# Kernel optimization log

Measured on AMD Instinct MI355X. Metric: run time of the kernel, lower is better.

The kernel has to match this reference:

```python
import jax, jax.numpy as jnp
import numpy as np

B, T, C, H = 4, 2048, 1024, 16
D = C // H  # head_dim = 64
SCALE = D ** -0.5


def setup_inputs() -> dict:
    key = jax.random.key(0)
    ks = jax.random.split(key, 5)
    s = C ** -0.5
    return {
        "x": jax.random.normal(ks[0], (B, T, C), dtype=jnp.float32),
        "W_qkv": jax.random.normal(ks[1], (C, 3 * C), dtype=jnp.float32) * s,
        "b_qkv": jnp.zeros((3 * C,), dtype=jnp.float32),
        "W_out": jax.random.normal(ks[2], (C, C), dtype=jnp.float32) * s,
        "b_out": jnp.zeros((C,), dtype=jnp.float32),
    }


def reference(x, W_qkv, b_qkv, W_out, b_out):
    Bx, Tx, Cx = x.shape
    qkv = x @ W_qkv + b_qkv                      # [B,T,3C]
    qkv = qkv.reshape(Bx, Tx, 3, H, D)
    q, k, v = qkv[:, :, 0], qkv[:, :, 1], qkv[:, :, 2]  # [B,T,H,D]
    # scores [B,H,T,T]
    scores = jnp.einsum("bthd,bshd->bhts", q, k) * SCALE
    causal = jnp.tril(jnp.ones((Tx, Tx), dtype=bool))
    scores = jnp.where(causal[None, None], scores, -jnp.inf)
    probs = jax.nn.softmax(scores, axis=-1)
    out = jnp.einsum("bhts,bshd->bthd", probs, v).reshape(Bx, Tx, Cx)
    return out @ W_out + b_out
```

## Files before the change

### kernel.cpp

```cpp
#include <hip/hip_runtime.h>
#include <cstdint>
#include <cstddef>

#define B_ 4
#define T_ 2048
#define C_ 1024
#define H_ 16
#define D_ 64
#define SCALE_ 0.125f

typedef _Float16 f16;
typedef f16 f16x4 __attribute__((ext_vector_type(4)));
typedef f16 f16x8 __attribute__((ext_vector_type(8)));
typedef float f32x4 __attribute__((ext_vector_type(4)));

__device__ __forceinline__ void async_ld16(const void* g, void* l) {
  __builtin_amdgcn_global_load_lds(
      (const __attribute__((address_space(1))) void*)g,
      (__attribute__((address_space(3))) void*)l,
      16, 0, 0);
}

__global__ void k_prep(const float* __restrict__ x, f16* __restrict__ xh,
                       const float* __restrict__ Wqkv, f16* __restrict__ WqkvT,
                       const float* __restrict__ Wout, f16* __restrict__ WoutT)
{
  __shared__ float tile[32][33];
  const int bx = blockIdx.x, t = threadIdx.x;
  if (bx < 8192) {
    int i = bx * 256 + t;
    float4 v = ((const float4*)x)[i];
    f16x4 h;
    h.x = (f16)v.x; h.y = (f16)v.y; h.z = (f16)v.z; h.w = (f16)v.w;
    ((f16x4*)xh)[i] = h;
    return;
  }
  const float* in; f16* out; int K, N, nt, kt;
  if (bx < 8192 + 3072) {
    int idx = bx - 8192; in = Wqkv; out = WqkvT; K = 1024; N = 3072;
    nt = idx % 96; kt = idx / 96;
  } else {
    int idx = bx - 11264; in = Wout; out = WoutT; K = 1024; N = 1024;
    nt = idx % 32; kt = idx / 32;
  }
  int tx = t & 31, ty = t >> 5;
  int k0 = kt * 32, n0 = nt * 32;
#pragma unroll
  for (int i = 0; i < 32; i += 8)
    tile[ty + i][tx] = in[(size_t)(k0 + ty + i) * N + n0 + tx];
  __syncthreads();
#pragma unroll
  for (int i = 0; i < 32; i += 8)
    out[(size_t)(n0 + ty + i) * K + k0 + tx] = (f16)tile[tx][ty + i];
}

__global__ void k_vtrans(const f16* __restrict__ QKV, f16* __restrict__ Vt) {
  __shared__ f16 tile[32][33];
  int tx = threadIdx.x & 31, ty = threadIdx.x >> 5;
  int t0 = blockIdx.x * 32, d0 = blockIdx.y * 32;
  int bh = blockIdx.z, b = bh >> 4, h = bh & 15;
#pragma unroll
  for (int i = 0; i < 32; i += 8)
    tile[ty + i][tx] = QKV[(size_t)(b * T_ + t0 + ty + i) * (3 * C_) + 2 * C_ + h * D_ + d0 + tx];
  __syncthreads();
#pragma unroll
  for (int i = 0; i < 32; i += 8)
    Vt[((size_t)bh * D_ + d0 + ty + i) * T_ + t0 + tx] = tile[tx][ty + i];
}

__global__ __launch_bounds__(256, 3)
void k_gemm_bt(const f16* __restrict__ A, const f16* __restrict__ Bt,
               const float* __restrict__ bias, f16* __restrict__ Ch,
               float* __restrict__ Cf, int M, int N, int K)
{
  __shared__ __align__(16) f16 As[2][128 * 32];
  __shared__ __align__(16) f16 Bs[2][128 * 32];
  const int t = threadIdx.x;
  const int wave = t >> 6, lane = t & 63, lr = lane & 15, quad = lane >> 4;
  const int row0 = blockIdx.y * 128, col0 = blockIdx.x * 128;
  const int wm = (wave >> 1) * 64, wn = (wave & 1) * 64;

  f32x4 acc[4][4] = {};

  const int sw = ((t & 3) ^ ((t >> 4) & 3)) * 8;
  const f16* gA = A + (size_t)(row0 + (t >> 2)) * K + sw;
  const f16* gB = Bt + (size_t)(col0 + (t >> 2)) * K + sw;
  const size_t rowskip = (size_t)64 * K;
  const int rc = (quad ^ (lr >> 2)) * 8;

  {
    f16* lA = As[0] + wave * 512;
    f16* lB = Bs[0] + wave * 512;
    async_ld16(gA,           lA);
    async_ld16(gA + rowskip, lA + 2048);
    async_ld16(gB,           lB);
    async_ld16(gB + rowskip, lB + 2048);
  }

  const int iters = K >> 5;
  for (int it = 0; it < iters; ++it) {
    __syncthreads();
    const int buf = it & 1;
    if (it + 1 < iters) {
      const int k0 = (it + 1) * 32;
      f16* lA = As[buf ^ 1] + wave * 512;
      f16* lB = Bs[buf ^ 1] + wave * 512;
      async_ld16(gA + k0,           lA);
      async_ld16(gA + rowskip + k0, lA + 2048);
      async_ld16(gB + k0,           lB);
      async_ld16(gB + rowskip + k0, lB + 2048);
    }
    const f16* As_ = As[buf];
    const f16* Bs_ = Bs[buf];

    f16x8 af[4], bf[4];
#pragma unroll
    for (int i = 0; i < 4; ++i) {
      af[i] = *(const f16x8*)&As_[(wm + i * 16 + lr) * 32 + rc];
      bf[i] = *(const f16x8*)&Bs_[(wn + i * 16 + lr) * 32 + rc];
    }
#pragma unroll
    for (int mi = 0; mi < 4; ++mi)
#pragma unroll
      for (int ni = 0; ni < 4; ++ni)
        acc[mi][ni] = __builtin_amdgcn_mfma_f32_16x16x32_f16(af[mi], bf[ni], acc[mi][ni], 0, 0, 0);
  }

#pragma unroll
  for (int mi = 0; mi < 4; ++mi) {
#pragma unroll
    for (int ni = 0; ni < 4; ++ni) {
      int col = col0 + wn + ni * 16 + lr;
      float bv = bias[col];
#pragma unroll
      for (int r = 0; r < 4; ++r) {
        int row = row0 + wm + mi * 16 + quad * 4 + r;
        float v = acc[mi][ni][r] + bv;
        if (Ch) Ch[(size_t)row * N + col] = (f16)v;
        else    Cf[(size_t)row * N + col] = v;
      }
    }
  }
}

__global__ __launch_bounds__(256, 4)
void k_flash(const f16* __restrict__ QKV, const f16* __restrict__ Vt, f16* __restrict__ O)
{
  __shared__ __align__(16) f16 Ks[2][64 * 64];
  __shared__ __align__(16) f16 Vs[2][64 * 64];
  __shared__ __align__(16) f16 Ps[4][16 * 64];

  const int a = blockIdx.x, bh = blockIdx.y;
  const int b = bh >> 4, h = bh & 15;
  const int qtA = a, qtB = 31 - a;
  const int t = threadIdx.x, wave = t >> 6, lane = t & 63, lr = lane & 15, quad = lane >> 4;
  const int lr3 = lr & 7;
  const int c0 = quad ^ lr3;
  const int c1 = c0 ^ 4;

  const f16 scl = (f16)0.125f;
  const f16* qpA = QKV + (size_t)(b * T_ + qtA * 64 + wave * 16 + lr) * 3072 + h * 64;
  const f16* qpB = QKV + (size_t)(b * T_ + qtB * 64 + wave * 16 + lr) * 3072 + h * 64;
  f16x8 qA0 = *(const f16x8*)(qpA + quad * 8)      * scl;
  f16x8 qA1 = *(const f16x8*)(qpA + 32 + quad * 8) * scl;
  f16x8 qB0 = *(const f16x8*)(qpB + quad * 8)      * scl;
  f16x8 qB1 = *(const f16x8*)(qpB + 32 + quad * 8) * scl;

  float lA_[4] = {0.f, 0.f, 0.f, 0.f};
  float lB_[4] = {0.f, 0.f, 0.f, 0.f};
  f32x4 oA[4] = {}, oB[4] = {};

  const int sw = ((t & 7) ^ ((t >> 3) & 7)) * 8;
  const f16* gK = QKV + (size_t)(b * T_ + (t >> 3)) * 3072 + 1024 + h * 64 + sw;
  const f16* gV = Vt + ((size_t)bh * 64 + (t >> 3)) * T_ + sw;

  f16* myP = Ps[wave];
  f16* pw0 = myP + (quad * 4) * 64 + ((0 ^ quad) << 4) + lr;
  f16* pw1 = myP + (quad * 4) * 64 + ((1 ^ quad) << 4) + lr;
  f16* pw2 = myP + (quad * 4) * 64 + ((2 ^ quad) << 4) + lr;
  f16* pw3 = myP + (quad * 4) * 64 + ((3 ^ quad) << 4) + lr;
  const f16* pr0 = myP + lr * 64 + ((((quad >> 1))     ^ (lr >> 2)) << 4) + ((quad & 1) << 3);
  const f16* pr1 = myP + lr * 64 + ((((quad >> 1) ^ 2) ^ (lr >> 2)) << 4) + ((quad & 1) << 3);

  const int last = qtB;

  {
    f16* lK = Ks[0] + wave * 512;
    f16* lV = Vs[0] + wave * 512;
    async_ld16(gK,                     lK);
    async_ld16(gK + (size_t)32 * 3072, lK + 2048);
    async_ld16(gV,                     lV);
    async_ld16(gV + (size_t)32 * T_,   lV + 2048);
  }

  for (int kt = 0; kt <= last; ++kt) {
    __syncthreads();
    const int buf = kt & 1;
    if (kt < last) {
      const f16* gk = gK + (size_t)((kt + 1) * 64) * 3072;
      const f16* gv = gV + (kt + 1) * 64;
      f16* lK = Ks[buf ^ 1] + wave * 512;
      f16* lV = Vs[buf ^ 1] + wave * 512;
      async_ld16(gk,                     lK);
      async_ld16(gk + (size_t)32 * 3072, lK + 2048);
      async_ld16(gv,                     lV);
      async_ld16(gv + (size_t)32 * T_,   lV + 2048);
    }
    const f16* K_ = Ks[buf];
    const f16* V_ = Vs[buf];
    const bool actA = (kt <= qtA);

    {
      f32x4 s4[4];
#pragma unroll
      for (int ni = 0; ni < 4; ++ni) {
        const f16* kr = K_ + (ni * 16 + lr) * 64;
        f16x8 k0 = *(const f16x8*)(kr + c0 * 8);
        f16x8 k1 = *(const f16x8*)(kr + c1 * 8);
        f32x4 z = {};
        z = __builtin_amdgcn_mfma_f32_16x16x32_f16(qB0, k0, z, 0, 0, 0);
        z = __builtin_amdgcn_mfma_f32_16x16x32_f16(qB1, k1, z, 0, 0, 0);
        s4[ni] = z;
      }
      if (kt == qtB) {
        const int rloc = wave * 16 + quad * 4;
#pragma unroll
        for (int r = 0; r < 4; ++r) {
#pragma unroll
          for (int ni = 0; ni < 4; ++ni)
            if (ni * 16 + lr > rloc + r) s4[ni][r] = -1e30f;
        }
      }
#pragma unroll
      for (int r = 0; r < 4; ++r) {
        float e0 = __expf(s4[0][r]), e1 = __expf(s4[1][r]);
        float e2 = __expf(s4[2][r]), e3 = __expf(s4[3][r]);
        lB_[r] += (e0 + e1) + (e2 + e3);
        pw0[r * 64] = (f16)e0; pw1[r * 64] = (f16)e1;
        pw2[r * 64] = (f16)e2; pw3[r * 64] = (f16)e3;
      }
      f16x8 pB0 = *(const f16x8*)pr0;
      f16x8 pB1 = *(const f16x8*)pr1;
#pragma unroll
      for (int ni = 0; ni < 4; ++ni) {
        const f16* vr = V_ + (ni * 16 + lr) * 64;
        f16x8 v0 = *(const f16x8*)(vr + c0 * 8);
        f16x8 v1 = *(const f16x8*)(vr + c1 * 8);
        oB[ni] = __builtin_amdgcn_mfma_f32_16x16x32_f16(pB0, v0, oB[ni], 0, 0, 0);
        oB[ni] = __builtin_amdgcn_mfma_f32_16x16x32_f16(pB1, v1, oB[ni], 0, 0, 0);
      }
    }

    if (actA) {
      f32x4 s4[4];
#pragma unroll
      for (int ni = 0; ni < 4; ++ni) {
        const f16* kr = K_ + (ni * 16 + lr) * 64;
        f16x8 k0 = *(const f16x8*)(kr + c0 * 8);
        f16x8 k1 = *(const f16x8*)(kr + c1 * 8);
        f32x4 z = {};
        z = __builtin_amdgcn_mfma_f32_16x16x32_f16(qA0, k0, z, 0, 0, 0);
        z = __builtin_amdgcn_mfma_f32_16x16x32_f16(qA1, k1, z, 0, 0, 0);
        s4[ni] = z;
      }
      if (kt == qtA) {
        const int rloc = wave * 16 + quad * 4;
#pragma unroll
        for (int r = 0; r < 4; ++r) {
#pragma unroll
          for (int ni = 0; ni < 4; ++ni)
            if (ni * 16 + lr > rloc + r) s4[ni][r] = -1e30f;
        }
      }
#pragma unroll
      for (int r = 0; r < 4; ++r) {
        float e0 = __expf(s4[0][r]), e1 = __expf(s4[1][r]);
        float e2 = __expf(s4[2][r]), e3 = __expf(s4[3][r]);
        lA_[r] += (e0 + e1) + (e2 + e3);
        pw0[r * 64] = (f16)e0; pw1[r * 64] = (f16)e1;
        pw2[r * 64] = (f16)e2; pw3[r * 64] = (f16)e3;
      }
      f16x8 pA0 = *(const f16x8*)pr0;
      f16x8 pA1 = *(const f16x8*)pr1;
#pragma unroll
      for (int ni = 0; ni < 4; ++ni) {
        const f16* vr = V_ + (ni * 16 + lr) * 64;
        f16x8 v0 = *(const f16x8*)(vr + c0 * 8);
        f16x8 v1 = *(const f16x8*)(vr + c1 * 8);
        oA[ni] = __builtin_amdgcn_mfma_f32_16x16x32_f16(pA0, v0, oA[ni], 0, 0, 0);
        oA[ni] = __builtin_amdgcn_mfma_f32_16x16x32_f16(pA1, v1, oA[ni], 0, 0, 0);
      }
    }
  }

#pragma unroll
  for (int r = 0; r < 4; ++r) {
    float la = lA_[r], lb = lB_[r];
#pragma unroll
    for (int off = 1; off < 16; off <<= 1) {
      la += __shfl_xor(la, off, 64);
      lb += __shfl_xor(lb, off, 64);
    }
    const int rowA = qtA * 64 + wave * 16 + quad * 4 + r;
    const int rowB = qtB * 64 + wave * 16 + quad * 4 + r;
    float invA = 1.f / la;
    float invB = 1.f / lb;
#pragma unroll
    for (int ni = 0; ni < 4; ++ni) {
      O[(size_t)(b * T_ + rowA) * C_ + h * 64 + ni * 16 + lr] = (f16)(oA[ni][r] * invA);
      O[(size_t)(b * T_ + rowB) * C_ + h * 64 + ni * 16 + lr] = (f16)(oB[ni][r] * invB);
    }
  }
}

extern "C" void kernel_launch(void* const* d_in, const int* in_sizes, int n_in,
                              void* d_out, int out_size, void* d_ws, size_t ws_size,
                              hipStream_t stream)
{
  const float* x    = (const float*)d_in[0];
  const float* Wqkv = (const float*)d_in[1];
  const float* bqkv = (const float*)d_in[2];
  const float* Wout = (const float*)d_in[3];
  const float* bout = (const float*)d_in[4];
  float* out = (float*)d_out;

  f16* xh    = (f16*)d_ws;
  f16* WqkvT = xh + (size_t)8192 * 1024;
  f16* WoutT = WqkvT + (size_t)3072 * 1024;
  f16* QKV   = WoutT + (size_t)1024 * 1024;
  f16* VtG   = QKV + (size_t)8192 * 3072;
  f16* Oh    = VtG + (size_t)64 * 64 * 2048;

  k_prep<<<12288, 256, 0, stream>>>(x, xh, Wqkv, WqkvT, Wout, WoutT);

  k_gemm_bt<<<dim3(3072 / 128, 8192 / 128), 256, 0, stream>>>(
      xh, WqkvT, bqkv, QKV, nullptr, 8192, 3072, 1024);

  k_vtrans<<<dim3(T_ / 32, D_ / 32, B_ * H_), 256, 0, stream>>>(QKV, VtG);

  k_flash<<<dim3(16, B_ * H_), 256, 0, stream>>>(QKV, VtG, Oh);

  k_gemm_bt<<<dim3(1024 / 128, 8192 / 128), 256, 0, stream>>>(
      Oh, WoutT, bout, nullptr, out, 8192, 1024, 1024);
}
```

Before: 274.3 us.

## Fuse V transpose into QKV GEMM epilogue and load GEMM operands directly from global

Drops the separate V-transpose kernel by having the QKV GEMM write V columns straight into the transposed Vt layout in its epilogue. The GEMM main loop also stops staging tiles through LDS with async loads. Each wave now loads its MFMA fragments directly from global memory into registers, using a two-stage register double buffer over K. This saves a launch and a round trip of V through memory. In exchange, operand reuse across waves via shared memory is lost, so global/L2 traffic rises and the Vt stores become strided and uncoalesced.

After: 406.9 us. +48.3%, slower.

```diff
diff --git a/kernel.cpp b/kernel.cpp
--- a/kernel.cpp
+++ b/kernel.cpp
@@ -54,90 +54,86 @@
     out[(size_t)(n0 + ty + i) * K + k0 + tx] = (f16)tile[tx][ty + i];
 }
 
-__global__ void k_vtrans(const f16* __restrict__ QKV, f16* __restrict__ Vt) {
-  __shared__ f16 tile[32][33];
-  int tx = threadIdx.x & 31, ty = threadIdx.x >> 5;
-  int t0 = blockIdx.x * 32, d0 = blockIdx.y * 32;
-  int bh = blockIdx.z, b = bh >> 4, h = bh & 15;
-#pragma unroll
-  for (int i = 0; i < 32; i += 8)
-    tile[ty + i][tx] = QKV[(size_t)(b * T_ + t0 + ty + i) * (3 * C_) + 2 * C_ + h * D_ + d0 + tx];
-  __syncthreads();
-#pragma unroll
-  for (int i = 0; i < 32; i += 8)
-    Vt[((size_t)bh * D_ + d0 + ty + i) * T_ + t0 + tx] = tile[tx][ty + i];
-}
-
 __global__ __launch_bounds__(256, 3)
 void k_gemm_bt(const f16* __restrict__ A, const f16* __restrict__ Bt,
                const float* __restrict__ bias, f16* __restrict__ Ch,
-               float* __restrict__ Cf, int M, int N, int K)
+               float* __restrict__ Cf, f16* __restrict__ VtOut,
+               int M, int N, int K)
 {
-  __shared__ __align__(16) f16 As[2][128 * 32];
-  __shared__ __align__(16) f16 Bs[2][128 * 32];
   const int t = threadIdx.x;
   const int wave = t >> 6, lane = t & 63, lr = lane & 15, quad = lane >> 4;
   const int row0 = blockIdx.y * 128, col0 = blockIdx.x * 128;
   const int wm = (wave >> 1) * 64, wn = (wave & 1) * 64;
 
+  const f16* pa = A  + (size_t)(row0 + wm + lr) * K + quad * 8;
+  const f16* pb = Bt + (size_t)(col0 + wn + lr) * K + quad * 8;
+  const size_t rs = (size_t)16 * K;
+
   f32x4 acc[4][4] = {};
-
-  const int sw = ((t & 3) ^ ((t >> 4) & 3)) * 8;
-  const f16* gA = A + (size_t)(row0 + (t >> 2)) * K + sw;
-  const f16* gB = Bt + (size_t)(col0 + (t >> 2)) * K + sw;
-  const size_t rowskip = (size_t)64 * K;
-  const int rc = (quad ^ (lr >> 2)) * 8;
-
-  {
-    f16* lA = As[0] + wave * 512;
-    f16* lB = Bs[0] + wave * 512;
-    async_ld16(gA,           lA);
-    async_ld16(gA + rowskip, lA + 2048);
-    async_ld16(gB,           lB);
-    async_ld16(gB + rowskip, lB + 2048);
-  }
-
-  const int iters = K >> 5;
-  for (int it = 0; it < iters; ++it) {
-    __syncthreads();
-    const int buf = it & 1;
-    if (it + 1 < iters) {
-      const int k0 = (it + 1) * 32;
-      f16* lA = As[buf ^ 1] + wave * 512;
-      f16* lB = Bs[buf ^ 1] + wave * 512;
-      async_ld16(gA + k0,           lA);
-      async_ld16(gA + rowskip + k0, lA + 2048);
-      async_ld16(gB + k0,           lB);
-      async_ld16(gB + rowskip + k0, lB + 2048);
-    }
-    const f16* As_ = As[buf];
-    const f16* Bs_ = Bs[buf];
-
-    f16x8 af[4], bf[4];
+  f16x8 a0[4], b0[4], a1[4], b1[4];
+
+#pragma unroll
+  for (int i = 0; i < 4; ++i) {
+    a0[i] = *(const f16x8*)(pa + i * rs);
+    b0[i] = *(const f16x8*)(pb + i * rs);
+  }
+
+  for (int k0 = 0; k0 < K; k0 += 64) {
 #pragma unroll
     for (int i = 0; i < 4; ++i) {
-      af[i] = *(const f16x8*)&As_[(wm + i * 16 + lr) * 32 + rc];
-      bf[i] = *(const f16x8*)&Bs_[(wn + i * 16 + lr) * 32 + rc];
+      a1[i] = *(const f16x8*)(pa + i * rs + k0 + 32);
+      b1[i] = *(const f16x8*)(pb + i * rs + k0 + 32);
     }
 #pragma unroll
     for (int mi = 0; mi < 4; ++mi)
 #pragma unroll
       for (int ni = 0; ni < 4; ++ni)
-        acc[mi][ni] = __builtin_amdgcn_mfma_f32_16x16x32_f16(af[mi], bf[ni], acc[mi][ni], 0, 0, 0);
-  }
-
-#pragma unroll
-  for (int mi = 0; mi < 4; ++mi) {
+        acc[mi][ni] = __builtin_amdgcn_mfma_f32_16x16x32_f16(a0[mi], b0[ni], acc[mi][ni], 0, 0, 0);
+    if (k0 + 64 < K) {
+#pragma unroll
+      for (int i = 0; i < 4; ++i) {
+        a0[i] = *(const f16x8*)(pa + i * rs + k0 + 64);
+        b0[i] = *(const f16x8*)(pb + i * rs + k0 + 64);
+      }
+    }
+#pragma unroll
+    for (int mi = 0; mi < 4; ++mi)
+#pragma unroll
+      for (int ni = 0; ni < 4; ++ni)
+        acc[mi][ni] = __builtin_amdgcn_mfma_f32_16x16x32_f16(a1[mi], b1[ni], acc[mi][ni], 0, 0, 0);
+  }
+
+  if (VtOut != nullptr && col0 >= 2048) {
 #pragma unroll
     for (int ni = 0; ni < 4; ++ni) {
-      int col = col0 + wn + ni * 16 + lr;
-      float bv = bias[col];
-#pragma unroll
-      for (int r = 0; r < 4; ++r) {
-        int row = row0 + wm + mi * 16 + quad * 4 + r;
-        float v = acc[mi][ni][r] + bv;
-        if (Ch) Ch[(size_t)row * N + col] = (f16)v;
-        else    Cf[(size_t)row * N + col] = v;
+      const int cb = col0 + wn + ni * 16 - 2048;
+      const int h = cb >> 6;
+      const int dd = (cb & 63) + lr;
+      const float bv = bias[2048 + cb + lr];
+#pragma unroll
+      for (int mi = 0; mi < 4; ++mi) {
+#pragma unroll
+        for (int r = 0; r < 4; ++r) {
+          const int row = row0 + wm + mi * 16 + quad * 4 + r;
+          const int bb = row >> 11, tt = row & 2047;
+          VtOut[((size_t)(bb * 16 + h) * 64 + dd) * T_ + tt] = (f16)(acc[mi][ni][r] + bv);
+        }
+      }
+    }
+  } else {
+#pragma unroll
+    for (int mi = 0; mi < 4; ++mi) {
+#pragma unroll
+      for (int ni = 0; ni < 4; ++ni) {
+        int col = col0 + wn + ni * 16 + lr;
+        float bv = bias[col];
+#pragma unroll
+        for (int r = 0; r < 4; ++r) {
+          int row = row0 + wm + mi * 16 + quad * 4 + r;
+          float v = acc[mi][ni][r] + bv;
+          if (Ch) Ch[(size_t)row * N + col] = (f16)v;
+          else    Cf[(size_t)row * N + col] = v;
+        }
       }
     }
   }
@@ -334,12 +330,10 @@
   k_prep<<<12288, 256, 0, stream>>>(x, xh, Wqkv, WqkvT, Wout, WoutT);
 
   k_gemm_bt<<<dim3(3072 / 128, 8192 / 128), 256, 0, stream>>>(
-      xh, WqkvT, bqkv, QKV, nullptr, 8192, 3072, 1024);
-
-  k_vtrans<<<dim3(T_ / 32, D_ / 32, B_ * H_), 256, 0, stream>>>(QKV, VtG);
+      xh, WqkvT, bqkv, QKV, nullptr, VtG, 8192, 3072, 1024);
 
   k_flash<<<dim3(16, B_ * H_), 256, 0, stream>>>(QKV, VtG, Oh);
 
   k_gemm_bt<<<dim3(1024 / 128, 8192 / 128), 256, 0, stream>>>(
-      Oh, WoutT, bout, nullptr, out, 8192, 1024, 1024);
-}
+      Oh, WoutT, bout, nullptr, out, nullptr, 8192, 1024, 1024);
+}
```

## Fuse V transpose into QKV GEMM epilogue and enlarge tile to 256x128

Applied to the files above, without the earlier changes.

The QKV projection now uses a new GEMM kernel with 256x128 tiles (8x4 MFMA accumulators per wave) instead of 128x128, and blocks covering the V columns write their output directly in transposed [bh][d][t] layout. This removes the separate V-transpose kernel launch and its extra read and write of V. The cost is scattered 2-byte transposed stores in the epilogue, plus more registers per thread that may lower occupancy, and fewer blocks (768 vs 1536) in the grid.

Measured after the change: 261.8 us. 4.6% less time.

```diff
diff --git a/kernel.cpp b/kernel.cpp
--- a/kernel.cpp
+++ b/kernel.cpp
@@ -54,24 +54,106 @@
     out[(size_t)(n0 + ty + i) * K + k0 + tx] = (f16)tile[tx][ty + i];
 }
 
-__global__ void k_vtrans(const f16* __restrict__ QKV, f16* __restrict__ Vt) {
-  __shared__ f16 tile[32][33];
-  int tx = threadIdx.x & 31, ty = threadIdx.x >> 5;
-  int t0 = blockIdx.x * 32, d0 = blockIdx.y * 32;
-  int bh = blockIdx.z, b = bh >> 4, h = bh & 15;
-#pragma unroll
-  for (int i = 0; i < 32; i += 8)
-    tile[ty + i][tx] = QKV[(size_t)(b * T_ + t0 + ty + i) * (3 * C_) + 2 * C_ + h * D_ + d0 + tx];
-  __syncthreads();
-#pragma unroll
-  for (int i = 0; i < 32; i += 8)
-    Vt[((size_t)bh * D_ + d0 + ty + i) * T_ + t0 + tx] = tile[tx][ty + i];
+__global__ __launch_bounds__(256, 3)
+void k_gemm256(const f16* __restrict__ A, const f16* __restrict__ Bt,
+               const float* __restrict__ bias, f16* __restrict__ Ch,
+               f16* __restrict__ VtOut, int M, int N, int K)
+{
+  __shared__ __align__(16) f16 As[2][256 * 32];
+  __shared__ __align__(16) f16 Bs[2][128 * 32];
+  const int t = threadIdx.x;
+  const int wave = t >> 6, lane = t & 63, lr = lane & 15, quad = lane >> 4;
+  const int row0 = blockIdx.y * 256, col0 = blockIdx.x * 128;
+  const int wm = (wave >> 1) * 128, wn = (wave & 1) * 64;
+
+  f32x4 acc[8][4] = {};
+
+  const int sw = ((t & 3) ^ ((t >> 4) & 3)) * 8;
+  const f16* gA = A + (size_t)(row0 + (t >> 2)) * K + sw;
+  const f16* gB = Bt + (size_t)(col0 + (t >> 2)) * K + sw;
+  const size_t rowskip = (size_t)64 * K;
+  const int rc = (quad ^ (lr >> 2)) * 8;
+
+  {
+    f16* lA = As[0] + wave * 512;
+    f16* lB = Bs[0] + wave * 512;
+    async_ld16(gA,                lA);
+    async_ld16(gA + rowskip,      lA + 2048);
+    async_ld16(gA + 2 * rowskip,  lA + 4096);
+    async_ld16(gA + 3 * rowskip,  lA + 6144);
+    async_ld16(gB,                lB);
+    async_ld16(gB + rowskip,      lB + 2048);
+  }
+
+  const int iters = K >> 5;
+  for (int it = 0; it < iters; ++it) {
+    __syncthreads();
+    const int buf = it & 1;
+    if (it + 1 < iters) {
+      const int k0 = (it + 1) * 32;
+      f16* lA = As[buf ^ 1] + wave * 512;
+      f16* lB = Bs[buf ^ 1] + wave * 512;
+      async_ld16(gA + k0,               lA);
+      async_ld16(gA + rowskip + k0,     lA + 2048);
+      async_ld16(gA + 2 * rowskip + k0, lA + 4096);
+      async_ld16(gA + 3 * rowskip + k0, lA + 6144);
+      async_ld16(gB + k0,               lB);
+      async_ld16(gB + rowskip + k0,     lB + 2048);
+    }
+    const f16* As_ = As[buf];
+    const f16* Bs_ = Bs[buf];
+
+    f16x8 bf[4];
+#pragma unroll
+    for (int i = 0; i < 4; ++i)
+      bf[i] = *(const f16x8*)&Bs_[(wn + i * 16 + lr) * 32 + rc];
+#pragma unroll
+    for (int mi = 0; mi < 8; ++mi) {
+      f16x8 af = *(const f16x8*)&As_[(wm + mi * 16 + lr) * 32 + rc];
+#pragma unroll
+      for (int ni = 0; ni < 4; ++ni)
+        acc[mi][ni] = __builtin_amdgcn_mfma_f32_16x16x32_f16(af, bf[ni], acc[mi][ni], 0, 0, 0);
+    }
+  }
+
+  if (VtOut != nullptr && col0 >= 2048) {
+#pragma unroll
+    for (int ni = 0; ni < 4; ++ni) {
+      const int cb = col0 + wn + ni * 16 - 2048;
+      const int h = cb >> 6;
+      const int dd = (cb & 63) + lr;
+      const float bv = bias[2048 + cb + lr];
+#pragma unroll
+      for (int mi = 0; mi < 8; ++mi) {
+#pragma unroll
+        for (int r = 0; r < 4; ++r) {
+          const int row = row0 + wm + mi * 16 + quad * 4 + r;
+          const int bb = row >> 11, tt = row & 2047;
+          VtOut[((size_t)(bb * 16 + h) * 64 + dd) * T_ + tt] = (f16)(acc[mi][ni][r] + bv);
+        }
+      }
+    }
+  } else {
+#pragma unroll
+    for (int mi = 0; mi < 8; ++mi) {
+#pragma unroll
+      for (int ni = 0; ni < 4; ++ni) {
+        int col = col0 + wn + ni * 16 + lr;
+        float bv = bias[col];
+#pragma unroll
+        for (int r = 0; r < 4; ++r) {
+          int row = row0 + wm + mi * 16 + quad * 4 + r;
+          Ch[(size_t)row * N + col] = (f16)(acc[mi][ni][r] + bv);
+        }
+      }
+    }
+  }
 }
 
 __global__ __launch_bounds__(256, 3)
 void k_gemm_bt(const f16* __restrict__ A, const f16* __restrict__ Bt,
-               const float* __restrict__ bias, f16* __restrict__ Ch,
-               float* __restrict__ Cf, int M, int N, int K)
+               const float* __restrict__ bias, float* __restrict__ Cf,
+               int M, int N, int K)
 {
   __shared__ __align__(16) f16 As[2][128 * 32];
   __shared__ __align__(16) f16 Bs[2][128 * 32];
@@ -135,9 +217,7 @@
 #pragma unroll
       for (int r = 0; r < 4; ++r) {
         int row = row0 + wm + mi * 16 + quad * 4 + r;
-        float v = acc[mi][ni][r] + bv;
-        if (Ch) Ch[(size_t)row * N + col] = (f16)v;
-        else    Cf[(size_t)row * N + col] = v;
+        Cf[(size_t)row * N + col] = acc[mi][ni][r] + bv;
       }
     }
   }
@@ -333,13 +413,11 @@
 
   k_prep<<<12288, 256, 0, stream>>>(x, xh, Wqkv, WqkvT, Wout, WoutT);
 
-  k_gemm_bt<<<dim3(3072 / 128, 8192 / 128), 256, 0, stream>>>(
-      xh, WqkvT, bqkv, QKV, nullptr, 8192, 3072, 1024);
-
-  k_vtrans<<<dim3(T_ / 32, D_ / 32, B_ * H_), 256, 0, stream>>>(QKV, VtG);
+  k_gemm256<<<dim3(3072 / 128, 8192 / 256), 256, 0, stream>>>(
+      xh, WqkvT, bqkv, QKV, VtG, 8192, 3072, 1024);
 
   k_flash<<<dim3(16, B_ * H_), 256, 0, stream>>>(QKV, VtG, Oh);
 
   k_gemm_bt<<<dim3(1024 / 128, 8192 / 128), 256, 0, stream>>>(
-      Oh, WoutT, bout, nullptr, out, 8192, 1024, 1024);
-}
+      Oh, WoutT, bout, out, 8192, 1024, 1024);
+}
```
